# Kernel optimization log

Measured on AMD Instinct MI355X. Metric: run time of the kernel, lower is better.

## Reference

```python
import jax, jax.numpy as jnp
import numpy as np

K = 3          # kernel_size
PAD = K // 2   # unfold padding
BN_EPS = 1e-5


def _conv(x, w, dilation, pad):
    # x: [B,C,H,W], w: [O,I,kh,kw]
    return jax.lax.conv_general_dilated(
        x, w, window_strides=(1, 1), padding=[(pad, pad), (pad, pad)],
        rhs_dilation=(dilation, dilation),
        dimension_numbers=("NCHW", "OIHW", "NCHW"))


def _bn(x, g, b, rm, rv):
    # eval-mode batchnorm with running stats
    inv = g / jnp.sqrt(rv + BN_EPS)
    return x * inv[None, :, None, None] + (b - rm * inv)[None, :, None, None]


def setup_inputs() -> dict:
    key = jax.random.key(0)
    ks = jax.random.split(key, 8)
    B, T, H, W = 8, 5, 512, 512
    mid = 16  # max(16, T // 4)
    inp = {
        "x_aligned": jax.random.normal(ks[0], (B, T, H, W), jnp.float32),
        "raw_diff": jax.random.normal(ks[1], (B, T - 1, H, W), jnp.float32),
        "w1": jax.random.normal(ks[2], (mid, T, 3, 3), jnp.float32) * 0.1,
        "g1": jnp.ones((mid,), jnp.float32), "b1": jnp.zeros((mid,), jnp.float32),
        "rm1": jnp.zeros((mid,), jnp.float32), "rv1": jnp.ones((mid,), jnp.float32),
        "w2": jax.random.normal(ks[3], (mid, mid, 3, 3), jnp.float32) * 0.1,
        "g2": jnp.ones((mid,), jnp.float32), "b2": jnp.zeros((mid,), jnp.float32),
        "rm2": jnp.zeros((mid,), jnp.float32), "rv2": jnp.ones((mid,), jnp.float32),
        "w3": jax.random.normal(ks[4], (mid, mid, 3, 3), jnp.float32) * 0.1,
        "g3": jnp.ones((mid,), jnp.float32), "b3": jnp.zeros((mid,), jnp.float32),
        "rm3": jnp.zeros((mid,), jnp.float32), "rv3": jnp.ones((mid,), jnp.float32),
        "w4": jax.random.normal(ks[5], (T * K * K, mid, 1, 1), jnp.float32) * 0.1,
        "bias": jnp.full((1,), -1.0, jnp.float32),
    }
    return inp


def reference(x_aligned, raw_diff, w1, g1, b1, rm1, rv1, w2, g2, b2, rm2, rv2,
              w3, g3, b3, rm3, rv3, w4, bias):
    B, T, H, W = x_aligned.shape
    # _accumulate: sequential abs-add == sum of abs over frame-diff axis
    acc = jnp.sum(jnp.abs(raw_diff), axis=1, keepdims=True)  # [B,1,H,W]
    mean = jnp.mean(acc)
    n = acc.size
    std = jnp.sqrt(jnp.sum((acc - mean) ** 2) / (n - 1))  # unbiased (torch default)
    motion = (acc - mean) / (std + 1e-6)
    motion_seq = jnp.broadcast_to(motion, (B, T, H, W))
    # _generate_kernel: conv+BN+ReLU stack with dilations 1,2,4 then 1x1
    h = jax.nn.relu(_bn(_conv(motion_seq, w1, 1, 1), g1, b1, rm1, rv1))
    h = jax.nn.relu(_bn(_conv(h, w2, 2, 2), g2, b2, rm2, rv2))
    h = jax.nn.relu(_bn(_conv(h, w3, 4, 4), g3, b3, rm3, rv3))
    raw_kernel = _conv(h, w4, 1, 0).reshape(B, T, K * K, H, W)
    kernel = (jax.nn.sigmoid(raw_kernel + bias[0]) + 0.01) * 10.0
    # _enhance: unfold (KxK patches, zero pad) then per-pixel weighted sum
    xp = jnp.pad(x_aligned, ((0, 0), (0, 0), (PAD, PAD), (PAD, PAD)))
    patches = jnp.stack(
        [xp[:, :, i:i + H, j:j + W] for i in range(K) for j in range(K)],
        axis=2)  # [B,T,K*K,H,W], matches F.unfold row-major kernel order
    return jnp.sum(kernel * patches, axis=2)  # [B,T,H,W]
```

## Files before the change

kernel.cpp:

```cpp
#include <hip/hip_runtime.h>
#include <hip/hip_bf16.h>
#include <math.h>

#define HH 512
#define WW 512
#define BB 8
#define TT 5
#define MID 16
#define HWSZ (HH*WW)
#define NPIX (BB*HWSZ)

typedef __attribute__((ext_vector_type(8))) short bf16x8;
typedef __attribute__((ext_vector_type(4))) short bf16x4;
typedef __attribute__((ext_vector_type(4))) float f32x4;

#if __has_builtin(__builtin_amdgcn_exp2f)
#define EXP2F(x) __builtin_amdgcn_exp2f(x)
#else
#define EXP2F(x) exp2f(x)
#endif

#define LOG2E 1.4426950408889634f

__device__ inline unsigned short f2bf(float f){
  unsigned u = __float_as_uint(f);
  u = u + 0x7fffu + ((u >> 16) & 1u);
  return (unsigned short)(u >> 16);
}
__device__ inline unsigned packpair(float a, float b){
  unsigned ua = __float_as_uint(a) + 0x8000u;
  unsigned ub = __float_as_uint(b) + 0x8000u;
  return __builtin_amdgcn_perm(ub, ua, 0x07060302u);
}
__device__ inline float blo(unsigned u){ return __uint_as_float(u << 16); }
__device__ inline float bhi(unsigned u){ return __uint_as_float(u & 0xffff0000u); }

union U4B { uint4 u; bf16x8 h; };
union U2B { uint2 u; bf16x4 h; };


__global__ __launch_bounds__(256) void k_acc(const float* __restrict__ rd,
                                             float4* __restrict__ acc,
                                             float2* __restrict__ partial){
  int t = blockIdx.x * 256 + threadIdx.x;
  int i = t << 2;
  int b = i >> 18, p = i & (HWSZ - 1);
  const float* base = rd + (size_t)b * 4 * HWSZ + p;
  float4 f0 = *(const float4*)(base);
  float4 f1 = *(const float4*)(base + HWSZ);
  float4 f2 = *(const float4*)(base + 2*HWSZ);
  float4 f3 = *(const float4*)(base + 3*HWSZ);
  float4 s4;
  s4.x = fabsf(f0.x) + fabsf(f1.x) + fabsf(f2.x) + fabsf(f3.x);
  s4.y = fabsf(f0.y) + fabsf(f1.y) + fabsf(f2.y) + fabsf(f3.y);
  s4.z = fabsf(f0.z) + fabsf(f1.z) + fabsf(f2.z) + fabsf(f3.z);
  s4.w = fabsf(f0.w) + fabsf(f1.w) + fabsf(f2.w) + fabsf(f3.w);
  acc[t] = s4;
  float s  = s4.x + s4.y + s4.z + s4.w;
  float s2 = s4.x*s4.x + s4.y*s4.y + s4.z*s4.z + s4.w*s4.w;
  #pragma unroll
  for (int off = 32; off; off >>= 1){
    s  += __shfl_down(s,  off);
    s2 += __shfl_down(s2, off);
  }
  __shared__ float ls[4], ls2[4];
  int lane = threadIdx.x & 63, wid = threadIdx.x >> 6;
  if (lane == 0){ ls[wid] = s; ls2[wid] = s2; }
  __syncthreads();
  if (threadIdx.x == 0)
    partial[blockIdx.x] = make_float2(ls[0]+ls[1]+ls[2]+ls[3],
                                      ls2[0]+ls2[1]+ls2[2]+ls2[3]);
}

__global__ __launch_bounds__(256) void k_prep(const float2* __restrict__ partial,
    const float* __restrict__ w1, const float* __restrict__ w2, const float* __restrict__ w3,
    const float* __restrict__ g1, const float* __restrict__ b1, const float* __restrict__ rm1, const float* __restrict__ rv1,
    const float* __restrict__ g2, const float* __restrict__ b2, const float* __restrict__ rm2, const float* __restrict__ rv2,
    const float* __restrict__ g3, const float* __restrict__ b3, const float* __restrict__ rm3, const float* __restrict__ rv3,
    const float* __restrict__ w4, const float* __restrict__ bias0,
    float* __restrict__ cst, unsigned* __restrict__ wsB2, unsigned* __restrict__ wsB3,
    uint2* __restrict__ wsB4){
  int t = threadIdx.x;
  double s = 0.0, s2 = 0.0;
  for (int j = t; j < 2048; j += 256){
    float2 v = partial[j];
    s += (double)v.x; s2 += (double)v.y;
  }
  #pragma unroll
  for (int off = 32; off; off >>= 1){
    s  += __shfl_down(s,  off);
    s2 += __shfl_down(s2, off);
  }
  __shared__ double ds[4], ds2[4];
  int lane = t & 63, wid = t >> 6;
  if (lane == 0){ ds[wid] = s; ds2[wid] = s2; }
  __syncthreads();
  if (t == 0){
    double S  = ds[0]+ds[1]+ds[2]+ds[3];
    double S2 = ds2[0]+ds2[1]+ds2[2]+ds2[3];
    double n = (double)NPIX;
    double mean = S / n;
    double var  = (S2 - n * mean * mean) / (n - 1.0);
    double sd   = sqrt(var);
    cst[0] = (float)mean;
    cst[1] = (float)(1.0 / (sd + 1e-6));
    cst[242] = bias0[0] * LOG2E;
  }
  if (t < 144){
    int c = t / 9, k = t % 9;
    float sw = 0.f;
    for (int f = 0; f < TT; f++) sw += w1[c*45 + f*9 + k];
    cst[2 + t] = sw;
  }
  if (t < 16){
    float s1 = g1[t] * rsqrtf(rv1[t] + 1e-5f);
    cst[146 + t] = s1; cst[162 + t] = b1[t] - rm1[t] * s1;
    float c2 = g2[t] * rsqrtf(rv2[t] + 1e-5f);
    cst[288 + t] = c2; cst[304 + t] = b2[t] - rm2[t] * c2;
    float c3 = g3[t] * rsqrtf(rv3[t] + 1e-5f);
    cst[320 + t] = c3; cst[336 + t] = b3[t] - rm3[t] * c3;
  }
  for (int it = 0; it < 5; it++){
    int idx = it * 256 + t;
    int m = idx >> 8, rem = idx & 255;
    int L = rem >> 2, jj = rem & 3;
    int out = L & 15, q = L >> 4;
    unsigned v2 = 0, v3 = 0;
    #pragma unroll
    for (int h = 0; h < 2; h++){
      int j = 2*jj + h;
      int k = q*8 + j;
      int tap = 2*m + (k >> 4);
      int ci = k & 15;
      unsigned bv2 = 0, bv3 = 0;
      if (tap < 9){
        bv2 = f2bf(w2[out*144 + ci*9 + tap]);
        bv3 = f2bf(w3[out*144 + ci*9 + tap]);
      }
      v2 |= bv2 << (16*h);
      v3 |= bv3 << (16*h);
    }
    wsB2[idx] = v2; wsB3[idx] = v3;
  }
  if (t < 192){
    int c = t >> 6, L = t & 63;
    int n = L & 15, q = L >> 4;
    int o = c*16 + n;
    unsigned pk0 = 0, pk1 = 0;
    if (o < 45){
      unsigned b0 = f2bf(w4[o*16 + q*4 + 0] * LOG2E);
      unsigned b1v = f2bf(w4[o*16 + q*4 + 1] * LOG2E);
      unsigned b2v = f2bf(w4[o*16 + q*4 + 2] * LOG2E);
      unsigned b3v = f2bf(w4[o*16 + q*4 + 3] * LOG2E);
      pk0 = b0 | (b1v << 16);
      pk1 = b2v | (b3v << 16);
    }
    wsB4[c*64 + L] = make_uint2(pk0, pk1);
  }
}

#define TR 12
#define TC 68
__global__ __launch_bounds__(256) void k_conv12(const float* __restrict__ acc,
                                                const float* __restrict__ C,
                                                const unsigned* __restrict__ wsB2,
                                                uint2* __restrict__ h2){
  __shared__ float AT[14*72];
  __shared__ uint4 PL[2][TR*TC];
  int tid = threadIdx.x;
  int blk = blockIdx.x;
  int xt = blk & 7, yt = (blk >> 3) & 63, b = blk >> 9;
  int y0 = yt << 3, x0 = xt << 6;
  float mean = C[0], inv = C[1];
  const float* ab = acc + ((size_t)b << 18);
  #pragma unroll
  for (int it = 0; it < 4; it++){
    int idx = it*256 + tid;
    if (idx < 14*72){
      int r = (idx * 1821) >> 17;
      int p = idx - r*72;
      int gy = y0 - 3 + r, gx = x0 - 3 + p;
      float v = 0.f;
      if ((unsigned)gy < HH && (unsigned)gx < WW)
        v = (ab[(gy << 9) + gx] - mean) * inv;
      AT[idx] = v;
    }
  }
  __syncthreads();
  #pragma unroll
  for (int it = 0; it < 4; it++){
    int i = it*256 + tid;
    if (i < TR*TC){
      int r2 = (i * 241) >> 14;
      int p2 = i - r2*TC;
      int gy = y0 - 2 + r2, gx = x0 - 2 + p2;
      uint4 lo = make_uint4(0u,0u,0u,0u), hi = lo;
      if ((unsigned)gy < HH && (unsigned)gx < WW){
        float a[MID];
        #pragma unroll
        for (int o = 0; o < MID; o++) a[o] = 0.f;
        #pragma unroll
        for (int ky = 0; ky < 3; ky++){
          #pragma unroll
          for (int kx = 0; kx < 3; kx++){
            float m = AT[(r2 + ky)*72 + (p2 + kx)];
            int k = ky * 3 + kx;
            #pragma unroll
            for (int o = 0; o < MID; o++) a[o] = fmaf(C[2 + o*9 + k], m, a[o]);
          }
        }
        unsigned pk[8];
        #pragma unroll
        for (int j = 0; j < 8; j++){
          float v0 = fmaxf(0.f, fmaf(a[2*j],   C[146 + 2*j],   C[162 + 2*j]));
          float v1 = fmaxf(0.f, fmaf(a[2*j+1], C[146 + 2*j+1], C[162 + 2*j+1]));
          pk[j] = packpair(v0, v1);
        }
        lo = make_uint4(pk[0], pk[1], pk[2], pk[3]);
        hi = make_uint4(pk[4], pk[5], pk[6], pk[7]);
      }
      PL[0][r2*TC + p2] = lo;
      PL[1][r2*TC + p2] = hi;
    }
  }
  __syncthreads();
  int lane = tid & 63, wv = tid >> 6;
  int col = lane & 15, q = lane >> 4;
  int chSel = q & 1;
  bool hiTap = (q >= 2);
  uint4 wfrag[5];
  #pragma unroll
  for (int m = 0; m < 5; m++) wfrag[m] = ((const uint4*)wsB2)[m*64 + lane];
  float4 sc = *(const float4*)&C[288 + q*4];
  float4 bi = *(const float4*)&C[304 + q*4];
  #pragma unroll
  for (int rr = 0; rr < 2; rr++){
    int ly = wv*2 + rr;
    #pragma unroll
    for (int g = 0; g < 4; g++){
      int lx = g << 4;
      f32x4 cc = {0.f, 0.f, 0.f, 0.f};
      #pragma unroll
      for (int m = 0; m < 5; m++){
        const int ta = 2*m, tb = (2*m + 1 > 8) ? 8 : (2*m + 1);
        int dy = (hiTap ? tb/3 : ta/3) - 1;
        int dx = (hiTap ? tb%3 : ta%3) - 1;
        int trow = ly + 2 + 2*dy;
        int tpx  = lx + 2 + col + 2*dx;
        U4B bv; bv.u = PL[chSel][trow*TC + tpx];
        U4B wb; wb.u = wfrag[m];
        cc = __builtin_amdgcn_mfma_f32_16x16x32_bf16(wb.h, bv.h, cc, 0, 0, 0);
      }
      float v0 = fmaxf(0.f, fmaf(cc[0], sc.x, bi.x));
      float v1 = fmaxf(0.f, fmaf(cc[1], sc.y, bi.y));
      float v2 = fmaxf(0.f, fmaf(cc[2], sc.z, bi.z));
      float v3 = fmaxf(0.f, fmaf(cc[3], sc.w, bi.w));
      int gy = y0 + ly, gx = x0 + lx + col;
      h2[(size_t)((b << 18) | (gy << 9) | gx)*4 + q] =
          make_uint2(packpair(v0, v1), packpair(v2, v3));
    }
  }
}

template<bool EDGE>
__device__ inline f32x4 convW4(const uint4* __restrict__ hin, const uint4 wfrag[5],
                               int b, int y, int x0, int col, int q, f32x4 cc){
  int chSel = q & 1;
  bool hiTap = (q >= 2);
  #pragma unroll
  for (int m = 0; m < 5; m++){
    const int ta = 2*m, tb = (2*m + 1 > 8) ? 8 : (2*m + 1);
    int dy = (hiTap ? tb/3 : ta/3) - 1;
    int dx = (hiTap ? tb%3 : ta%3) - 1;
    int yy = y + dy * 4;
    int xx = x0 + col + dx * 4;
    U4B a;
    if (EDGE){
      bool valid = ((unsigned)yy < HH) && ((unsigned)xx < WW);
      a.u = make_uint4(0u, 0u, 0u, 0u);
      if (valid) a.u = hin[(((unsigned)((b << 18) | (yy << 9) | xx)) << 1) | (unsigned)chSel];
    } else {
      a.u = hin[(((unsigned)((b << 18) | (yy << 9) | xx)) << 1) | (unsigned)chSel];
    }
    U4B bb; bb.u = wfrag[m];
    cc = __builtin_amdgcn_mfma_f32_16x16x32_bf16(bb.h, a.h, cc, 0, 0, 0);
  }
  return cc;
}

__device__ __forceinline__ void stage2_tail(int g, f32x4 cc, float4 sc, float4 bi,
    float cb, const uint2 bw4[3], char* myL, int q, int col){
  float v0 = fmaxf(0.f, fmaf(cc[0], sc.x, bi.x));
  float v1 = fmaxf(0.f, fmaf(cc[1], sc.y, bi.y));
  float v2 = fmaxf(0.f, fmaf(cc[2], sc.z, bi.z));
  float v3 = fmaxf(0.f, fmaf(cc[3], sc.w, bi.w));
  U2B bb;
  bb.u.x = packpair(v0, v1);
  bb.u.y = packpair(v2, v3);
  char* wp = myL + (g*16 + col)*104 + q*8;
  #pragma unroll
  for (int c = 0; c < 3; c++){
    f32x4 aw = {cb, cb, cb, cb};
    U2B af; af.u = bw4[c];
    aw = __builtin_amdgcn_mfma_f32_16x16x16bf16_1k(af.h, bb.h, aw, 0, 0, 0);
    float k0 = fmaf(10.f, __builtin_amdgcn_rcpf(1.f + EXP2F(-aw[0])), 0.1f);
    float k1 = fmaf(10.f, __builtin_amdgcn_rcpf(1.f + EXP2F(-aw[1])), 0.1f);
    float k2 = fmaf(10.f, __builtin_amdgcn_rcpf(1.f + EXP2F(-aw[2])), 0.1f);
    float k3 = fmaf(10.f, __builtin_amdgcn_rcpf(1.f + EXP2F(-aw[3])), 0.1f);
    *(uint2*)(wp + c*32) = make_uint2(packpair(k0, k1), packpair(k2, k3));
  }
}

__global__ __launch_bounds__(256, 3) void k_conv3m(const uint4* __restrict__ h2,
                                                   const float* __restrict__ C,
                                                   const unsigned* __restrict__ wsB3,
                                                   const uint2* __restrict__ wsB4,
                                                   const float* __restrict__ xal,
                                                   float* __restrict__ out){
  __shared__ uint2 LB[4][832];
  int lane = threadIdx.x & 63, wv = threadIdx.x >> 6;
  char* myL = (char*)LB[wv];
  int w = blockIdx.x * 4 + wv;
  int base = w << 6;
  int b = base >> 18, rem = base & (HWSZ - 1);
  int y = rem >> 9, wx = rem & 511;
  uint4 wfrag[5];
  #pragma unroll
  for (int m = 0; m < 5; m++) wfrag[m] = ((const uint4*)wsB3)[m*64 + lane];
  uint2 bw4[3];
  #pragma unroll
  for (int c = 0; c < 3; c++) bw4[c] = wsB4[c*64 + lane];
  int col = lane & 15, q = lane >> 4;
  int chSel = q & 1;
  bool hiTap = (q >= 2);
  float4 sc = *(const float4*)&C[320 + q*4];
  float4 bi = *(const float4*)&C[336 + q*4];
  float cb = C[242];

  bool f1 = (y >= 4) && (y < 508) && (wx >= 64) && (wx <= 384);
  if (f1){
    const int dyA[5] = {-1,-1,0,1,1}, dyB[5] = {-1,0,0,1,1};
    const int dxA[5] = {-1,1,0,-1,1}, dxB[5] = {0,-1,1,0,1};
    const char* hb = (const char*)h2
        + ((((size_t)b << 18) + (unsigned)(y << 9)) << 5)
        + ((unsigned)(wx + col) << 5) + (chSel << 4);
    const char* pmt[5];
    #pragma unroll
    for (int m = 0; m < 5; m++){
      int off = hiTap ? (dyB[m]*65536 + dxB[m]*128)
                      : (dyA[m]*65536 + dxA[m]*128);
      pmt[m] = hb + off;
    }
    uint4 tap[4][5];
    #pragma unroll
    for (int g = 0; g < 4; g++){
      #pragma unroll
      for (int m = 0; m < 5; m++)
        tap[g][m] = *(const uint4*)(pmt[m] + g*512);
    }
    #pragma unroll
    for (int g = 0; g < 4; g++){
      f32x4 cc = {0.f, 0.f, 0.f, 0.f};
      #pragma unroll
      for (int m = 0; m < 5; m++){
        U4B bv; bv.u = tap[g][m];
        U4B wb; wb.u = wfrag[m];
        cc = __builtin_amdgcn_mfma_f32_16x16x32_bf16(wb.h, bv.h, cc, 0, 0, 0);
      }
      stage2_tail(g, cc, sc, bi, cb, bw4, myL, q, col);
    }
  } else {
    bool yIn = (y >= 4) && (y < 508);
    #pragma unroll
    for (int g = 0; g < 4; g++){
      int x0 = wx + g*16;
      f32x4 cc = {0.f, 0.f, 0.f, 0.f};
      bool fast = yIn && (x0 >= 4) && (x0 <= 492);
      if (fast) cc = convW4<false>(h2, wfrag, b, y, x0, col, q, cc);
      else      cc = convW4<true >(h2, wfrag, b, y, x0, col, q, cc);
      stage2_tail(g, cc, sc, bi, cb, bw4, myL, q, col);
    }
  }

  unsigned kvf[24];
  {
    const uint2* kp = (const uint2*)(myL + lane*104);
    #pragma unroll
    for (int jj = 0; jj < 12; jj++){
      uint2 u = kp[jj];
      kvf[2*jj] = u.x; kvf[2*jj+1] = u.y;
    }
  }
  int px = wx + lane;
  bool f3 = (y > 0) && (y < 511) && (wx != 0) && (wx != 448);
  if (f3){
    const char* p0 = (const char*)xal + (((size_t)(b*TT)) << 20)
                   + (unsigned)(y << 11) + (px << 2);
    #pragma unroll
    for (int t = 0; t < TT; t++){
      const char* pc = p0 + (size_t)t * (HWSZ*4);
      float xv[9];
      xv[0] = *(const float*)(pc - 2052);
      xv[1] = *(const float*)(pc - 2048);
      xv[2] = *(const float*)(pc - 2044);
      xv[3] = *(const float*)(pc - 4);
      xv[4] = *(const float*)(pc);
      xv[5] = *(const float*)(pc + 4);
      xv[6] = *(const float*)(pc + 2044);
      xv[7] = *(const float*)(pc + 2048);
      xv[8] = *(const float*)(pc + 2052);
      float ov = 0.f;
      #pragma unroll
      for (int k = 0; k < 9; k++){
        int n = t*9 + k;
        unsigned u = kvf[n >> 1];
        float kf = (n & 1) ? bhi(u) : blo(u);
        ov = fmaf(kf, xv[k], ov);
      }
      out[((size_t)(b*TT + t) << 18) + (y << 9) + px] = ov;
    }
  } else {
    bool mxl = (px > 0), mxr = (px < 511), mym = (y > 0), myp = (y < 511);
    bool msk[9] = { mym&&mxl, mym, mym&&mxr,
                    mxl,      true, mxr,
                    myp&&mxl, myp, myp&&mxr };
    int rowm = mym ? -2048 : 0;
    int rowp = myp ?  2048 : 0;
    int loff = mxl ? -4 : 0;
    int roff = mxr ?  4 : 0;
    const char* base0 = (const char*)(xal + ((size_t)(b*TT) << 18) + (y << 9) + px);
    #pragma unroll
    for (int t = 0; t < TT; t++){
      const char* pc = base0 + (size_t)t * (HWSZ*4);
      const char* pm = pc + rowm;
      const char* pp = pc + rowp;
      float xv[9];
      xv[0] = *(const float*)(pm + loff);
      xv[1] = *(const float*)(pm);
      xv[2] = *(const float*)(pm + roff);
      xv[3] = *(const float*)(pc + loff);
      xv[4] = *(const float*)(pc);
      xv[5] = *(const float*)(pc + roff);
      xv[6] = *(const float*)(pp + loff);
      xv[7] = *(const float*)(pp);
      xv[8] = *(const float*)(pp + roff);
      float ov = 0.f;
      #pragma unroll
      for (int k = 0; k < 9; k++){
        int n = t*9 + k;
        unsigned u = kvf[n >> 1];
        float kf = (n & 1) ? bhi(u) : blo(u);
        float kern = msk[k] ? kf : 0.f;
        ov = fmaf(kern, xv[k], ov);
      }
      out[((size_t)(b*TT + t) << 18) + (y << 9) + px] = ov;
    }
  }
}

extern "C" void kernel_launch(void* const* d_in, const int* in_sizes, int n_in,
                              void* d_out, int out_size, void* d_ws, size_t ws_size,
                              hipStream_t stream){
  const float* xal = (const float*)d_in[0];
  const float* rd  = (const float*)d_in[1];
  const float* w1  = (const float*)d_in[2];
  const float* g1  = (const float*)d_in[3];
  const float* b1  = (const float*)d_in[4];
  const float* rm1 = (const float*)d_in[5];
  const float* rv1 = (const float*)d_in[6];
  const float* w2  = (const float*)d_in[7];
  const float* g2  = (const float*)d_in[8];
  const float* b2  = (const float*)d_in[9];
  const float* rm2 = (const float*)d_in[10];
  const float* rv2 = (const float*)d_in[11];
  const float* w3  = (const float*)d_in[12];
  const float* g3  = (const float*)d_in[13];
  const float* b3  = (const float*)d_in[14];
  const float* rm3 = (const float*)d_in[15];
  const float* rv3 = (const float*)d_in[16];
  const float* w4  = (const float*)d_in[17];
  const float* bias= (const float*)d_in[18];
  float* out = (float*)d_out;

  char* ws = (char*)d_ws;
  float2*   partial = (float2*)ws;
  float*    cst   = (float*)(ws + 16384);
  unsigned* wsB2  = (unsigned*)(ws + 32768);
  unsigned* wsB3  = (unsigned*)(ws + 40960);
  uint2*    wsB4  = (uint2*)(ws + 49152);
  float*    acc   = (float*)(ws + 65536);
  char*     h2    = (char*)(ws + 65536 + (size_t)NPIX*4);

  k_acc<<<2048, 256, 0, stream>>>(rd, (float4*)acc, partial);
  k_prep<<<1, 256, 0, stream>>>(partial, w1, w2, w3,
                                g1, b1, rm1, rv1,
                                g2, b2, rm2, rv2,
                                g3, b3, rm3, rv3, w4, bias, cst, wsB2, wsB3, wsB4);
  k_conv12<<<4096, 256, 0, stream>>>(acc, cst, wsB2, (uint2*)h2);
  k_conv3m<<<NPIX/256, 256, 0, stream>>>((const uint4*)h2, cst, wsB3, wsB4, xal, out);
}
```

Before: 246.4 us.

## Fold prep into acc kernel, reduce stats per block, use MFMA for conv1

Drops the single-block k_prep launch: weight packing moves into an extra block of k_acc, and each k_conv12 block now reduces the 2048 partial sums itself (in float instead of double) to get mean and inverse std. The first conv layer (collapsed to one channel over 9 taps) is now computed with a bf16 16x16x16 MFMA, with the BN scale folded into the weights, instead of scalar FMAs. The LDS plane layout is interleaved into a single array. Risks are redundant per-block reduction work, lower precision for the statistics and bf16 rounding of the first-layer inputs.

```diff
diff --git a/kernel.cpp b/kernel.cpp
--- a/kernel.cpp
+++ b/kernel.cpp
@@ -40,10 +40,82 @@
 
 
 __global__ __launch_bounds__(256) void k_acc(const float* __restrict__ rd,
-                                             float4* __restrict__ acc,
-                                             float2* __restrict__ partial){
-  int t = blockIdx.x * 256 + threadIdx.x;
-  int i = t << 2;
+    float4* __restrict__ acc, float2* __restrict__ partial,
+    const float* __restrict__ w1, const float* __restrict__ g1, const float* __restrict__ b1,
+    const float* __restrict__ rm1, const float* __restrict__ rv1,
+    const float* __restrict__ w2, const float* __restrict__ g2, const float* __restrict__ b2,
+    const float* __restrict__ rm2, const float* __restrict__ rv2,
+    const float* __restrict__ w3, const float* __restrict__ g3, const float* __restrict__ b3,
+    const float* __restrict__ rm3, const float* __restrict__ rv3,
+    const float* __restrict__ w4, const float* __restrict__ bias0,
+    float* __restrict__ cst, uint2* __restrict__ wsA1,
+    unsigned* __restrict__ wsB2, unsigned* __restrict__ wsB3, uint2* __restrict__ wsB4){
+  int t = threadIdx.x;
+  if (blockIdx.x == 2048){
+    if (t == 0) cst[242] = bias0[0] * LOG2E;
+    if (t < 16){
+      float s1 = g1[t] * rsqrtf(rv1[t] + 1e-5f);
+      cst[162 + t] = b1[t] - rm1[t] * s1;
+      float c2 = g2[t] * rsqrtf(rv2[t] + 1e-5f);
+      cst[288 + t] = c2; cst[304 + t] = b2[t] - rm2[t] * c2;
+      float c3 = g3[t] * rsqrtf(rv3[t] + 1e-5f);
+      cst[320 + t] = c3; cst[336 + t] = b3[t] - rm3[t] * c3;
+    }
+    if (t < 64){
+      int o = t & 15, qq = t >> 4;
+      float s1o = g1[o] * rsqrtf(rv1[o] + 1e-5f);
+      unsigned pk2[2];
+      #pragma unroll
+      for (int h = 0; h < 2; h++){
+        unsigned lo = 0, hi = 0;
+        int tp0 = qq*4 + 2*h, tp1 = tp0 + 1;
+        if (tp0 < 9){ float sw = 0.f; for (int f = 0; f < TT; f++) sw += w1[o*45 + f*9 + tp0]; lo = f2bf(sw * s1o); }
+        if (tp1 < 9){ float sw = 0.f; for (int f = 0; f < TT; f++) sw += w1[o*45 + f*9 + tp1]; hi = f2bf(sw * s1o); }
+        pk2[h] = lo | (hi << 16);
+      }
+      wsA1[t] = make_uint2(pk2[0], pk2[1]);
+    }
+    for (int it = 0; it < 5; it++){
+      int idx = it * 256 + t;
+      int m = idx >> 8, rem = idx & 255;
+      int L = rem >> 2, jj = rem & 3;
+      int out = L & 15, q = L >> 4;
+      unsigned v2 = 0, v3 = 0;
+      #pragma unroll
+      for (int h = 0; h < 2; h++){
+        int j = 2*jj + h;
+        int k = q*8 + j;
+        int tap = 2*m + (k >> 4);
+        int ci = k & 15;
+        unsigned bv2 = 0, bv3 = 0;
+        if (tap < 9){
+          bv2 = f2bf(w2[out*144 + ci*9 + tap]);
+          bv3 = f2bf(w3[out*144 + ci*9 + tap]);
+        }
+        v2 |= bv2 << (16*h);
+        v3 |= bv3 << (16*h);
+      }
+      wsB2[idx] = v2; wsB3[idx] = v3;
+    }
+    if (t < 192){
+      int c = t >> 6, L = t & 63;
+      int n = L & 15, q = L >> 4;
+      int o = c*16 + n;
+      unsigned pk0 = 0, pk1 = 0;
+      if (o < 45){
+        unsigned b0 = f2bf(w4[o*16 + q*4 + 0] * LOG2E);
+        unsigned b1v = f2bf(w4[o*16 + q*4 + 1] * LOG2E);
+        unsigned b2v = f2bf(w4[o*16 + q*4 + 2] * LOG2E);
+        unsigned b3v = f2bf(w4[o*16 + q*4 + 3] * LOG2E);
+        pk0 = b0 | (b1v << 16);
+        pk1 = b2v | (b3v << 16);
+      }
+      wsB4[c*64 + L] = make_uint2(pk0, pk1);
+    }
+    return;
+  }
+  int gt = blockIdx.x * 256 + t;
+  int i = gt << 2;
   int b = i >> 18, p = i & (HWSZ - 1);
   const float* base = rd + (size_t)b * 4 * HWSZ + p;
   float4 f0 = *(const float4*)(base);
@@ -55,7 +127,7 @@
   s4.y = fabsf(f0.y) + fabsf(f1.y) + fabsf(f2.y) + fabsf(f3.y);
   s4.z = fabsf(f0.z) + fabsf(f1.z) + fabsf(f2.z) + fabsf(f3.z);
   s4.w = fabsf(f0.w) + fabsf(f1.w) + fabsf(f2.w) + fabsf(f3.w);
-  acc[t] = s4;
+  acc[gt] = s4;
   float s  = s4.x + s4.y + s4.z + s4.w;
   float s2 = s4.x*s4.x + s4.y*s4.y + s4.z*s4.z + s4.w*s4.w;
   #pragma unroll
@@ -64,114 +136,51 @@
     s2 += __shfl_down(s2, off);
   }
   __shared__ float ls[4], ls2[4];
-  int lane = threadIdx.x & 63, wid = threadIdx.x >> 6;
+  int lane = t & 63, wid = t >> 6;
   if (lane == 0){ ls[wid] = s; ls2[wid] = s2; }
   __syncthreads();
-  if (threadIdx.x == 0)
+  if (t == 0)
     partial[blockIdx.x] = make_float2(ls[0]+ls[1]+ls[2]+ls[3],
                                       ls2[0]+ls2[1]+ls2[2]+ls2[3]);
-}
-
-__global__ __launch_bounds__(256) void k_prep(const float2* __restrict__ partial,
-    const float* __restrict__ w1, const float* __restrict__ w2, const float* __restrict__ w3,
-    const float* __restrict__ g1, const float* __restrict__ b1, const float* __restrict__ rm1, const float* __restrict__ rv1,
-    const float* __restrict__ g2, const float* __restrict__ b2, const float* __restrict__ rm2, const float* __restrict__ rv2,
-    const float* __restrict__ g3, const float* __restrict__ b3, const float* __restrict__ rm3, const float* __restrict__ rv3,
-    const float* __restrict__ w4, const float* __restrict__ bias0,
-    float* __restrict__ cst, unsigned* __restrict__ wsB2, unsigned* __restrict__ wsB3,
-    uint2* __restrict__ wsB4){
-  int t = threadIdx.x;
-  double s = 0.0, s2 = 0.0;
-  for (int j = t; j < 2048; j += 256){
-    float2 v = partial[j];
-    s += (double)v.x; s2 += (double)v.y;
-  }
-  #pragma unroll
-  for (int off = 32; off; off >>= 1){
-    s  += __shfl_down(s,  off);
-    s2 += __shfl_down(s2, off);
-  }
-  __shared__ double ds[4], ds2[4];
-  int lane = t & 63, wid = t >> 6;
-  if (lane == 0){ ds[wid] = s; ds2[wid] = s2; }
-  __syncthreads();
-  if (t == 0){
-    double S  = ds[0]+ds[1]+ds[2]+ds[3];
-    double S2 = ds2[0]+ds2[1]+ds2[2]+ds2[3];
-    double n = (double)NPIX;
-    double mean = S / n;
-    double var  = (S2 - n * mean * mean) / (n - 1.0);
-    double sd   = sqrt(var);
-    cst[0] = (float)mean;
-    cst[1] = (float)(1.0 / (sd + 1e-6));
-    cst[242] = bias0[0] * LOG2E;
-  }
-  if (t < 144){
-    int c = t / 9, k = t % 9;
-    float sw = 0.f;
-    for (int f = 0; f < TT; f++) sw += w1[c*45 + f*9 + k];
-    cst[2 + t] = sw;
-  }
-  if (t < 16){
-    float s1 = g1[t] * rsqrtf(rv1[t] + 1e-5f);
-    cst[146 + t] = s1; cst[162 + t] = b1[t] - rm1[t] * s1;
-    float c2 = g2[t] * rsqrtf(rv2[t] + 1e-5f);
-    cst[288 + t] = c2; cst[304 + t] = b2[t] - rm2[t] * c2;
-    float c3 = g3[t] * rsqrtf(rv3[t] + 1e-5f);
-    cst[320 + t] = c3; cst[336 + t] = b3[t] - rm3[t] * c3;
-  }
-  for (int it = 0; it < 5; it++){
-    int idx = it * 256 + t;
-    int m = idx >> 8, rem = idx & 255;
-    int L = rem >> 2, jj = rem & 3;
-    int out = L & 15, q = L >> 4;
-    unsigned v2 = 0, v3 = 0;
-    #pragma unroll
-    for (int h = 0; h < 2; h++){
-      int j = 2*jj + h;
-      int k = q*8 + j;
-      int tap = 2*m + (k >> 4);
-      int ci = k & 15;
-      unsigned bv2 = 0, bv3 = 0;
-      if (tap < 9){
-        bv2 = f2bf(w2[out*144 + ci*9 + tap]);
-        bv3 = f2bf(w3[out*144 + ci*9 + tap]);
-      }
-      v2 |= bv2 << (16*h);
-      v3 |= bv3 << (16*h);
-    }
-    wsB2[idx] = v2; wsB3[idx] = v3;
-  }
-  if (t < 192){
-    int c = t >> 6, L = t & 63;
-    int n = L & 15, q = L >> 4;
-    int o = c*16 + n;
-    unsigned pk0 = 0, pk1 = 0;
-    if (o < 45){
-      unsigned b0 = f2bf(w4[o*16 + q*4 + 0] * LOG2E);
-      unsigned b1v = f2bf(w4[o*16 + q*4 + 1] * LOG2E);
-      unsigned b2v = f2bf(w4[o*16 + q*4 + 2] * LOG2E);
-      unsigned b3v = f2bf(w4[o*16 + q*4 + 3] * LOG2E);
-      pk0 = b0 | (b1v << 16);
-      pk1 = b2v | (b3v << 16);
-    }
-    wsB4[c*64 + L] = make_uint2(pk0, pk1);
-  }
 }
 
 #define TR 12
 #define TC 68
 __global__ __launch_bounds__(256) void k_conv12(const float* __restrict__ acc,
+                                                const float2* __restrict__ partial,
                                                 const float* __restrict__ C,
+                                                const uint2* __restrict__ wsA1,
                                                 const unsigned* __restrict__ wsB2,
                                                 uint2* __restrict__ h2){
-  __shared__ float AT[14*72];
-  __shared__ uint4 PL[2][TR*TC];
+  __shared__ struct {
+    float AT[14*72];
+    uint4 PLq[816*2];
+  } SM;
+  __shared__ float rs[4], rs2[4];
   int tid = threadIdx.x;
   int blk = blockIdx.x;
   int xt = blk & 7, yt = (blk >> 3) & 63, b = blk >> 9;
   int y0 = yt << 3, x0 = xt << 6;
-  float mean = C[0], inv = C[1];
+
+  float s = 0.f, s2 = 0.f;
+  for (int j = tid; j < 1024; j += 256){
+    float4 v = ((const float4*)partial)[j];
+    s += v.x + v.z; s2 += v.y + v.w;
+  }
+  #pragma unroll
+  for (int off = 32; off; off >>= 1){
+    s  += __shfl_down(s,  off);
+    s2 += __shfl_down(s2, off);
+  }
+  if ((tid & 63) == 0){ rs[tid >> 6] = s; rs2[tid >> 6] = s2; }
+  __syncthreads();
+  float S  = rs[0] + rs[1] + rs[2] + rs[3];
+  float S2 = rs2[0] + rs2[1] + rs2[2] + rs2[3];
+  float n = (float)NPIX;
+  float mean = S / n;
+  float var  = (S2 - n * mean * mean) / (n - 1.0f);
+  float inv  = 1.f / (sqrtf(var) + 1e-6f);
+
   const float* ab = acc + ((size_t)b << 18);
   #pragma unroll
   for (int it = 0; it < 4; it++){
@@ -183,49 +192,52 @@
       float v = 0.f;
       if ((unsigned)gy < HH && (unsigned)gx < WW)
         v = (ab[(gy << 9) + gx] - mean) * inv;
-      AT[idx] = v;
+      SM.AT[idx] = v;
     }
   }
   __syncthreads();
-  #pragma unroll
-  for (int it = 0; it < 4; it++){
-    int i = it*256 + tid;
-    if (i < TR*TC){
-      int r2 = (i * 241) >> 14;
-      int p2 = i - r2*TC;
-      int gy = y0 - 2 + r2, gx = x0 - 2 + p2;
-      uint4 lo = make_uint4(0u,0u,0u,0u), hi = lo;
-      if ((unsigned)gy < HH && (unsigned)gx < WW){
-        float a[MID];
-        #pragma unroll
-        for (int o = 0; o < MID; o++) a[o] = 0.f;
-        #pragma unroll
-        for (int ky = 0; ky < 3; ky++){
-          #pragma unroll
-          for (int kx = 0; kx < 3; kx++){
-            float m = AT[(r2 + ky)*72 + (p2 + kx)];
-            int k = ky * 3 + kx;
-            #pragma unroll
-            for (int o = 0; o < MID; o++) a[o] = fmaf(C[2 + o*9 + k], m, a[o]);
-          }
-        }
-        unsigned pk[8];
-        #pragma unroll
-        for (int j = 0; j < 8; j++){
-          float v0 = fmaxf(0.f, fmaf(a[2*j],   C[146 + 2*j],   C[162 + 2*j]));
-          float v1 = fmaxf(0.f, fmaf(a[2*j+1], C[146 + 2*j+1], C[162 + 2*j+1]));
-          pk[j] = packpair(v0, v1);
-        }
-        lo = make_uint4(pk[0], pk[1], pk[2], pk[3]);
-        hi = make_uint4(pk[4], pk[5], pk[6], pk[7]);
-      }
-      PL[0][r2*TC + p2] = lo;
-      PL[1][r2*TC + p2] = hi;
-    }
-  }
-  __syncthreads();
+
   int lane = tid & 63, wv = tid >> 6;
   int col = lane & 15, q = lane >> 4;
+
+  {
+    U2B a1; a1.u = wsA1[lane];
+    float4 b1v = *(const float4*)&C[162 + q*4];
+    f32x4 cinit = {b1v.x, b1v.y, b1v.z, b1v.w};
+    int off_[4];
+    #pragma unroll
+    for (int j = 0; j < 4; j++){
+      int tap = q*4 + j;
+      int ky = (tap*11) >> 5;
+      int kx = tap - 3*ky;
+      off_[j] = (ky*72 + kx)*4;
+    }
+    const char* ATb = (const char*)SM.AT;
+    char* PLb = (char*)SM.PLq;
+    for (int tt = wv; tt < 51; tt += 4){
+      int p = tt*16 + col;
+      int r2 = (p * 241) >> 14;
+      int p2 = p - r2*TC;
+      int bofs = (r2*72 + p2) * 4;
+      float m0 = *(const float*)(ATb + bofs + off_[0]);
+      float m1 = *(const float*)(ATb + bofs + off_[1]);
+      float m2 = *(const float*)(ATb + bofs + off_[2]);
+      float m3 = *(const float*)(ATb + bofs + off_[3]);
+      U2B bfr;
+      bfr.u.x = packpair(m0, m1);
+      bfr.u.y = packpair(m2, m3);
+      f32x4 z = __builtin_amdgcn_mfma_f32_16x16x16bf16_1k(a1.h, bfr.h, cinit, 0, 0, 0);
+      int gy = y0 - 2 + r2, gx = x0 - 2 + p2;
+      unsigned pk0 = 0u, pk1 = 0u;
+      if (((unsigned)gy < HH) && ((unsigned)gx < WW)){
+        pk0 = packpair(fmaxf(0.f, z[0]), fmaxf(0.f, z[1]));
+        pk1 = packpair(fmaxf(0.f, z[2]), fmaxf(0.f, z[3]));
+      }
+      *(uint2*)(PLb + p*32 + q*8) = make_uint2(pk0, pk1);
+    }
+  }
+  __syncthreads();
+
   int chSel = q & 1;
   bool hiTap = (q >= 2);
   uint4 wfrag[5];
@@ -247,7 +259,7 @@
         int dx = (hiTap ? tb%3 : ta%3) - 1;
         int trow = ly + 2 + 2*dy;
         int tpx  = lx + 2 + col + 2*dx;
-        U4B bv; bv.u = PL[chSel][trow*TC + tpx];
+        U4B bv; bv.u = SM.PLq[(unsigned)((trow*TC + tpx) << 1) | (unsigned)chSel];
         U4B wb; wb.u = wfrag[m];
         cc = __builtin_amdgcn_mfma_f32_16x16x32_bf16(wb.h, bv.h, cc, 0, 0, 0);
       }
@@ -488,14 +500,15 @@
   unsigned* wsB2  = (unsigned*)(ws + 32768);
   unsigned* wsB3  = (unsigned*)(ws + 40960);
   uint2*    wsB4  = (uint2*)(ws + 49152);
+  uint2*    wsA1  = (uint2*)(ws + 57344);
   float*    acc   = (float*)(ws + 65536);
   char*     h2    = (char*)(ws + 65536 + (size_t)NPIX*4);
 
-  k_acc<<<2048, 256, 0, stream>>>(rd, (float4*)acc, partial);
-  k_prep<<<1, 256, 0, stream>>>(partial, w1, w2, w3,
-                                g1, b1, rm1, rv1,
-                                g2, b2, rm2, rv2,
-                                g3, b3, rm3, rv3, w4, bias, cst, wsB2, wsB3, wsB4);
-  k_conv12<<<4096, 256, 0, stream>>>(acc, cst, wsB2, (uint2*)h2);
+  k_acc<<<2049, 256, 0, stream>>>(rd, (float4*)acc, partial,
+                                  w1, g1, b1, rm1, rv1,
+                                  w2, g2, b2, rm2, rv2,
+                                  w3, g3, b3, rm3, rv3,
+                                  w4, bias, cst, wsA1, wsB2, wsB3, wsB4);
+  k_conv12<<<4096, 256, 0, stream>>>(acc, partial, cst, wsA1, wsB2, (uint2*)h2);
   k_conv3m<<<NPIX/256, 256, 0, stream>>>((const uint4*)h2, cst, wsB3, wsB4, xal, out);
 }
```

Result: no change. 242.8 us (-1.4%).
